# Kernel optimization log

Hardware: AMD Instinct MI355X
Metric: run time of the kernel (lower is better)

The kernel has to match this reference:

```python
import jax, jax.numpy as jnp
import numpy as np

ALPHA = 0.9
EPS = 1e-6


def setup_inputs() -> dict:
    key = jax.random.key(0)
    k1, k2 = jax.random.split(key)
    T, B, D, n = 4096, 16, 1024, 64
    x = jax.random.normal(k1, (T, B, D), dtype=jnp.float32)
    S = jnp.zeros((B, n, n), dtype=jnp.float32)
    # xavier-uniform-ish scale for each [n, D] block of the fused projection
    bound = np.sqrt(6.0 / (n + D))
    W_kvq = jax.random.uniform(k2, (3 * n, D), dtype=jnp.float32, minval=-bound, maxval=bound)
    return {"x": x, "S": S, "W_kvq": W_kvq}


def _e74_forward(x, S0, W_kvq):
    T, B, D = x.shape
    n = W_kvq.shape[0] // 3
    # fused k, v, q projection: [T, B, 3n]
    proj = jnp.einsum('tbd,nd->tbn', x, W_kvq)
    k_all, v_all, q_all = proj[..., :n], proj[..., n:2 * n], proj[..., 2 * n:]

    def step(S, kvq):
        k, v, q = kvq  # each [B, n]
        k_norm = k / (jnp.linalg.norm(k, axis=-1, keepdims=True) + EPS)
        retrieved = jnp.einsum('bij,bj->bi', S, k_norm)
        delta = v - retrieved
        S = ALPHA * S + delta[:, :, None] * k_norm[:, None, :]
        Sq = jnp.einsum('bij,bj->bi', S, q)
        out = Sq * jax.nn.silu(Sq)
        return S, out

    S_final, outputs = jax.lax.scan(step, S0, (k_all, v_all, q_all))
    return outputs, S_final  # [T, B, n], [B, n, n]


def reference(x, S, W_kvq):
    return _e74_forward(x, S, W_kvq)
```

## Files before the change

### kernel.cpp

```cpp
#include <hip/hip_runtime.h>

#define ALPHA 0.9f
#define EPS 1e-6f
#define LOG2A  (-0.15200309344504995f)
#define A64F   (1.1790184577738583e-3f)

constexpr int T_DIM  = 4096;
constexpr int B_DIM  = 16;
constexpr int D_DIM  = 1024;
constexpr int N_DIM  = 64;
constexpr int NPROJ  = 192;
constexpr int NCHUNK = 64;

typedef float  f32x4   __attribute__((ext_vector_type(4)));
typedef _Float16 f16x8 __attribute__((ext_vector_type(8)));

__device__ __forceinline__ float powA(float e) {
  return exp2f(e * LOG2A);
}
__device__ __forceinline__ float rdlane(float v, int src) {
  return __builtin_bit_cast(float,
      __builtin_amdgcn_readlane(__builtin_bit_cast(int, v), src));
}

__device__ __constant__ float APOW[16] = {
  1.f, 0.9f, 0.81f, 0.729f, 0.6561f, 0.59049f, 0.531441f, 0.4782969f,
  0.43046721f, 0.387420489f, 0.3486784401f, 0.31381059609f,
  0.282429536481f, 0.2541865828329f, 0.22876792454961f, 0.205891132094649f};
__device__ __constant__ float AINV[16] = {
  1.f, 1.1111111111f, 1.2345679012f, 1.3717421125f, 1.5241579028f,
  1.6935087809f, 1.8816764232f, 2.0907515814f, 2.3230573126f,
  2.5811747918f, 2.8679719909f, 3.1866355454f, 3.5407061616f,
  3.9341179573f, 4.3712421748f, 4.8569357498f};

__global__ __launch_bounds__(256) void convert_w(
    const float* __restrict__ W, _Float16* __restrict__ w16)
{
  int i = blockIdx.x * 256 + threadIdx.x;
  int c = i >> 10, k = i & 1023;
  w16[(k >> 5) * (NPROJ * 32) + c * 32 + (k & 31)] = (_Float16)W[i];
}

constexpr int BM = 128, BK = 32, NS = D_DIM / BK;

__global__ __launch_bounds__(512, 2) void proj_gemm(
    const float* __restrict__ x, const _Float16* __restrict__ w16,
    _Float16* __restrict__ pf16)
{
  __shared__ _Float16 As[2][BM * BK];
  __shared__ _Float16 Bs[2][NPROJ * BK];
  __shared__ float    nrm[BM][2];

  const int tid  = threadIdx.x;
  const int w    = tid >> 6, lane = tid & 63;
  const int wr   = w >> 2, wc = w & 3;
  const int fr   = lane & 15, fg = lane >> 4;
  const int row0 = blockIdx.x * BM;

  const int arow = tid >> 2, akq = (tid & 3) * 8;
  const float* aSrc = x + (size_t)(row0 + arow) * D_DIM + akq;

  f32x4 acc[4][3];
#pragma unroll
  for (int i = 0; i < 4; ++i)
#pragma unroll
    for (int j = 0; j < 3; ++j) acc[i][j] = (f32x4){0.f, 0.f, 0.f, 0.f};

  float4 a0, a1;

  auto loadA = [&](int s) {
    const float* p = aSrc + s * BK;
    a0 = *(const float4*)p;
    a1 = *(const float4*)(p + 4);
  };
  auto writeA = [&](int buf) {
    f16x8 h;
    h[0] = (_Float16)a0.x; h[1] = (_Float16)a0.y;
    h[2] = (_Float16)a0.z; h[3] = (_Float16)a0.w;
    h[4] = (_Float16)a1.x; h[5] = (_Float16)a1.y;
    h[6] = (_Float16)a1.z; h[7] = (_Float16)a1.w;
    *(f16x8*)&As[buf][arow * BK + akq] = h;
  };
  auto stageB = [&](int buf, int s) {
#pragma unroll
    for (int j = 0; j < 2; ++j) {
      const int sl = j * 8 + w;
      if (sl < 12) {
        const _Float16* src = w16 + (size_t)s * (NPROJ * 32) + sl * 512;
        __builtin_amdgcn_global_load_lds(
            (const __attribute__((address_space(1))) unsigned int*)(src) + lane * 4,
            (__attribute__((address_space(3))) unsigned int*)&Bs[buf][sl * 512],
            16, 0, 0);
      }
    }
  };
  auto compute = [&](int buf) {
    f16x8 af[4];
#pragma unroll
    for (int ar = 0; ar < 4; ++ar)
      af[ar] = *(const f16x8*)&As[buf][(wr * 64 + ar * 16 + fr) * BK + fg * 8];
#pragma unroll
    for (int bc = 0; bc < 3; ++bc) {
      f16x8 bf = *(const f16x8*)&Bs[buf][(wc * 48 + bc * 16 + fr) * BK + fg * 8];
#pragma unroll
      for (int ar = 0; ar < 4; ++ar)
        acc[ar][bc] = __builtin_amdgcn_mfma_f32_16x16x32_f16(af[ar], bf, acc[ar][bc], 0, 0, 0);
    }
  };

  loadA(0);
  stageB(0, 0);
  writeA(0);
  __syncthreads();

  int buf = 0;
  for (int s = 0; s < NS; ++s) {
    if (s + 1 < NS) {
      loadA(s + 1);
      stageB(buf ^ 1, s + 1);
    }
    compute(buf);
    if (s + 1 < NS) writeA(buf ^ 1);
    __syncthreads();
    buf ^= 1;
  }

  if (wc < 2) {
#pragma unroll
    for (int ar = 0; ar < 4; ++ar)
#pragma unroll
      for (int r = 0; r < 4; ++r) {
        float ss;
        if (wc == 0) {
          const float p0 = acc[ar][0][r], p1 = acc[ar][1][r], p2 = acc[ar][2][r];
          ss = p0 * p0 + p1 * p1 + p2 * p2;
        } else {
          const float p0 = acc[ar][0][r];
          ss = p0 * p0;
        }
        ss += __shfl_xor(ss, 1, 64);
        ss += __shfl_xor(ss, 2, 64);
        ss += __shfl_xor(ss, 4, 64);
        ss += __shfl_xor(ss, 8, 64);
        if (fr == 0) nrm[wr * 64 + ar * 16 + fg * 4 + r][wc] = ss;
      }
  }
  __syncthreads();
  if (wc < 2) {
#pragma unroll
    for (int ar = 0; ar < 4; ++ar)
#pragma unroll
      for (int r = 0; r < 4; ++r) {
        const int row = wr * 64 + ar * 16 + fg * 4 + r;
        const float rn = 1.0f / (sqrtf(nrm[row][0] + nrm[row][1]) + EPS);
        if (wc == 0) {
          acc[ar][0][r] *= rn; acc[ar][1][r] *= rn; acc[ar][2][r] *= rn;
        } else {
          acc[ar][0][r] *= rn;
        }
      }
  }

#pragma unroll
  for (int ar = 0; ar < 4; ++ar) {
    const int row = row0 + wr * 64 + ar * 16 + fg * 4;
#pragma unroll
    for (int bc = 0; bc < 3; ++bc) {
      const int col = wc * 48 + bc * 16 + fr;
#pragma unroll
      for (int r = 0; r < 4; ++r)
        pf16[(size_t)(row + r) * NPROJ + col] = (_Float16)acc[ar][bc][r];
    }
  }
}

__global__ __launch_bounds__(64) void scan_sw(
    const _Float16* __restrict__ pf16, const float* __restrict__ S0,
    float* __restrict__ out, float* __restrict__ Sfin)
{
  __shared__ __align__(16) _Float16 sK[64][72];
  __shared__ __align__(16) _Float16 sQ[64][72];
  __shared__ __align__(16) _Float16 sV[64][72];
  __shared__ __align__(16) _Float16 sSW[64][72];
  __shared__ __align__(16) _Float16 sDT[64][80];
  __shared__ __align__(16) _Float16 sBB[16][72];
  __shared__ __align__(16) _Float16 sGt[16][40];

  const int lane = threadIdx.x;
  const int fr = lane & 15, fg = lane >> 4;
  const int b = blockIdx.x & (B_DIM - 1), c = blockIdx.x >> 4;
  const int t0o = c * 64;
  const bool c0 = (c == 0);

#pragma unroll
  for (int j = 0; j < 40; ++j) ((unsigned*)&sDT[0][0])[j * 64 + lane] = 0u;
#pragma unroll
  for (int j = 0; j < 5; ++j) ((unsigned*)&sGt[0][0])[j * 64 + lane] = 0u;

  auto stage64 = [&](_Float16 (*dst)[72], int t0, int sel) {
#pragma unroll
    for (int it = 0; it < 8; ++it) {
      int g = it * 64 + lane, t = g >> 3, c8 = g & 7;
      uint4 v = *(const uint4*)(pf16 + ((size_t)(t0 + t) * B_DIM + b) * NPROJ + sel + c8 * 8);
      *(uint4*)&dst[t][c8 * 8] = v;
    }
  };

  auto dotT = [&](const _Float16* A, int sa, int ra, const _Float16* B, int sb, int rb) {
    f32x4 a = (f32x4){0.f, 0.f, 0.f, 0.f};
    f16x8 af = *(const f16x8*)(A + (ra + fr) * sa + fg * 8);
    f16x8 bf = *(const f16x8*)(B + (rb + fr) * sb + fg * 8);
    a = __builtin_amdgcn_mfma_f32_16x16x32_f16(af, bf, a, 0, 0, 0);
    af = *(const f16x8*)(A + (ra + fr) * sa + 32 + fg * 8);
    bf = *(const f16x8*)(B + (rb + fr) * sb + 32 + fg * 8);
    a = __builtin_amdgcn_mfma_f32_16x16x32_f16(af, bf, a, 0, 0, 0);
    return a;
  };

  auto transposeK = [&]() {
    f16x8 rv[8];
#pragma unroll
    for (int q8 = 0; q8 < 8; ++q8) rv[q8] = *(const f16x8*)&sK[lane][q8 * 8];
#pragma unroll
    for (int q8 = 0; q8 < 8; ++q8)
#pragma unroll
      for (int e = 0; e < 8; ++e) sQ[q8 * 8 + e][lane] = rv[q8][e];
  };

  auto solve = [&](bool isW) {
    for (int k = 0; k < 4; ++k) {
      if (k > 0) {
        f32x4 bacc[4];
#pragma unroll
        for (int ib = 0; ib < 4; ++ib) bacc[ib] = (f32x4){0.f, 0.f, 0.f, 0.f};
        for (int j = 0; j < k; ++j) {
          f32x4 g = dotT(&sK[0][0], 72, k * 16, &sK[0][0], 72, j * 16);
#pragma unroll
          for (int r = 0; r < 4; ++r) {
            const int tl = fg * 4 + r;
            const float e = isW ? (float)(16 * k + tl - 64)
                                : (float)(16 * (k - j) + tl - fr - 1);
            sGt[tl][fr] = (_Float16)(g[r] * powA(e));
          }
#pragma unroll
          for (int ib = 0; ib < 4; ++ib) {
            f16x8 af = *(const f16x8*)&sGt[fr][fg * 8];
            f16x8 bf = *(const f16x8*)&sDT[ib * 16 + fr][j * 16 + fg * 8];
            bacc[ib] = __builtin_amdgcn_mfma_f32_16x16x32_f16(af, bf, bacc[ib], 0, 0, 0);
          }
        }
#pragma unroll
        for (int ib = 0; ib < 4; ++ib)
#pragma unroll
          for (int r = 0; r < 4; ++r)
            sBB[fg * 4 + r][ib * 16 + fr] = (_Float16)bacc[ib][r];
      }

      const f32x4 gd = dotT(&sK[0][0], 72, k * 16, &sK[0][0], 72, k * 16);

      float d[16], dA[16];
#pragma unroll
      for (int t = 0; t < 16; ++t) {
        float base = (float)sV[k * 16 + t][lane];
        if (k > 0) base -= (float)sBB[t][lane];
        float sum = 0.f;
#pragma unroll
        for (int tau = 0; tau < t; ++tau)
          sum = fmaf(rdlane(gd[t & 3], (t >> 2) * 16 + tau), dA[tau], sum);
        d[t] = (t == 0) ? base : fmaf(-APOW[t - 1], sum, base);
        dA[t] = d[t] * AINV[t];
      }
#pragma unroll
      for (int t8 = 0; t8 < 2; ++t8) {
        f16x8 pack;
#pragma unroll
        for (int e = 0; e < 8; ++e) {
          const int tl = t8 * 8 + e;
          const float sc = isW ? powA((float)(63 - (16 * k + tl))) : 1.f;
          pack[e] = (_Float16)(d[tl] * sc);
        }
        *(f16x8*)&sDT[lane][k * 16 + t8 * 8] = pack;
      }
    }
  };

  if (!c0) {
    stage64(sK, t0o - 64, 0);
    stage64(sV, t0o - 64, 64);
    solve(true);
    transposeK();
#pragma unroll
    for (int ti = 0; ti < 4; ++ti)
#pragma unroll
      for (int tj = 0; tj < 4; ++tj) {
        f32x4 a = dotT(&sDT[0][0], 80, ti * 16, &sQ[0][0], 72, tj * 16);
#pragma unroll
        for (int r = 0; r < 4; ++r)
          sSW[ti * 16 + fg * 4 + r][tj * 16 + fr] = (_Float16)a[r];
      }
  } else {
#pragma unroll
    for (int it = 0; it < 8; ++it) {
      const int row = it * 8 + (lane >> 3), col = (lane & 7) * 8;
      const float* src = S0 + (size_t)b * 4096 + row * 64 + col;
      const float4 v1 = *(const float4*)src;
      const float4 v2 = *(const float4*)(src + 4);
      f16x8 pk;
      pk[0] = (_Float16)v1.x; pk[1] = (_Float16)v1.y;
      pk[2] = (_Float16)v1.z; pk[3] = (_Float16)v1.w;
      pk[4] = (_Float16)v2.x; pk[5] = (_Float16)v2.y;
      pk[6] = (_Float16)v2.z; pk[7] = (_Float16)v2.w;
      *(f16x8*)&sSW[row][col] = pk;
    }
  }

  stage64(sK, t0o, 0);
  stage64(sQ, t0o, 128);
  stage64(sV, t0o, 64);

#pragma unroll
  for (int ti = 0; ti < 4; ++ti)
#pragma unroll
    for (int tj = 0; tj < 4; ++tj) {
      f32x4 a = dotT(&sK[0][0], 72, ti * 16, &sSW[0][0], 72, tj * 16);
#pragma unroll
      for (int r = 0; r < 4; ++r) {
        const int t = ti * 16 + fg * 4 + r, i = tj * 16 + fr;
        const float vo = (float)sV[t][i];
        sV[t][i] = (_Float16)(vo - powA((float)t) * a[r]);
      }
    }

  f32x4 sq[16];
#pragma unroll
  for (int ti = 0; ti < 4; ++ti)
#pragma unroll
    for (int tj = 0; tj < 4; ++tj) {
      f32x4 a = dotT(&sQ[0][0], 72, ti * 16, &sSW[0][0], 72, tj * 16);
#pragma unroll
      for (int r = 0; r < 4; ++r)
        a[r] *= powA((float)(ti * 16 + fg * 4 + r + 1));
      sq[ti * 4 + tj] = a;
    }

  solve(false);

#pragma unroll
  for (int tb = 0; tb < 4; ++tb)
#pragma unroll
    for (int qb = 0; qb < 4; ++qb) {
      if (qb <= tb) {
        f32x4 h = dotT(&sQ[0][0], 72, tb * 16, &sK[0][0], 72, qb * 16);
#pragma unroll
        for (int r = 0; r < 4; ++r) {
          const int tl = fg * 4 + r;
          const int t = tb * 16 + tl, tau = qb * 16 + fr;
          const float val = (tau <= t) ? h[r] * powA((float)(t - tau)) : 0.f;
          sGt[tl][fr] = (_Float16)val;
        }
#pragma unroll
        for (int ib = 0; ib < 4; ++ib) {
          f16x8 af = *(const f16x8*)&sGt[fr][fg * 8];
          f16x8 bf = *(const f16x8*)&sDT[ib * 16 + fr][qb * 16 + fg * 8];
          sq[tb * 4 + ib] = __builtin_amdgcn_mfma_f32_16x16x32_f16(af, bf, sq[tb * 4 + ib], 0, 0, 0);
        }
      }
    }

#pragma unroll
  for (int ti = 0; ti < 4; ++ti)
#pragma unroll
    for (int tj = 0; tj < 4; ++tj)
#pragma unroll
      for (int r = 0; r < 4; ++r) {
        const int t = ti * 16 + fg * 4 + r, i = tj * 16 + fr;
        const float Sq = sq[ti * 4 + tj][r];
        const float sig = 1.0f / (1.0f + __expf(-Sq));
        out[(size_t)(t0o + t) * 1024 + b * 64 + i] = Sq * Sq * sig;
      }

  if (c == NCHUNK - 1) {
#pragma unroll
    for (int t8 = 0; t8 < 8; ++t8) {
      f16x8 v = *(const f16x8*)&sDT[lane][t8 * 8];
#pragma unroll
      for (int e = 0; e < 8; ++e)
        v[e] = (_Float16)((float)v[e] * powA((float)(63 - (t8 * 8 + e))));
      *(f16x8*)&sDT[lane][t8 * 8] = v;
    }
    transposeK();
#pragma unroll
    for (int ti = 0; ti < 4; ++ti)
#pragma unroll
      for (int tj = 0; tj < 4; ++tj) {
        f32x4 so = dotT(&sDT[0][0], 80, ti * 16, &sQ[0][0], 72, tj * 16);
#pragma unroll
        for (int r = 0; r < 4; ++r) {
          const int i = ti * 16 + fg * 4 + r, j = tj * 16 + fr;
          Sfin[((size_t)b * 64 + i) * 64 + j] = A64F * (float)sSW[i][j] + so[r];
        }
      }
  }
}

extern "C" void kernel_launch(void* const* d_in, const int* in_sizes, int n_in,
                              void* d_out, int out_size, void* d_ws, size_t ws_size,
                              hipStream_t stream)
{
  const float* x  = (const float*)d_in[0];
  const float* S0 = (const float*)d_in[1];
  const float* Wk = (const float*)d_in[2];
  float* out  = (float*)d_out;
  float* Sfin = out + (size_t)T_DIM * B_DIM * N_DIM;

  char* wsb = (char*)d_ws;
  _Float16* pf16 = (_Float16*)(wsb);
  _Float16* w16  = (_Float16*)(wsb + 25165824);

  convert_w<<<(NPROJ * D_DIM) / 256, 256, 0, stream>>>(Wk, w16);
  proj_gemm<<<(T_DIM * B_DIM) / BM, 512, 0, stream>>>(x, w16, pf16);
  scan_sw<<<B_DIM * NCHUNK, 64, 0, stream>>>(pf16, S0, out, Sfin);
}
```

Before: 120.3 us.

## Stage GEMM epilogue through LDS and shrink scan kernel LDS and registers

The projection GEMM now stages its fp16 output tile through shared memory, reusing the operand buffers, so each thread writes 16-byte vectors instead of scattered 2-byte stores. In the scan kernel, V is read straight from global memory into registers inside the solve, and the K·S correction is folded into each solve block. Q is staged in two 32-row halves, the K transpose is done in place, and the output accumulators are kept per 16-row block instead of all 16 tiles. The forward-substitution dot product is split across four partial sums to shorten the dependency chain. Together these cut LDS footprint and register pressure to raise occupancy, at the cost of extra barriers and global loads inside the serial solve.

```diff
diff --git a/kernel.cpp b/kernel.cpp
--- a/kernel.cpp
+++ b/kernel.cpp
@@ -47,9 +47,12 @@
     const float* __restrict__ x, const _Float16* __restrict__ w16,
     _Float16* __restrict__ pf16)
 {
-  __shared__ _Float16 As[2][BM * BK];
-  __shared__ _Float16 Bs[2][NPROJ * BK];
-  __shared__ float    nrm[BM][2];
+  __shared__ __align__(16) _Float16 smem[2 * BM * BK + 2 * NPROJ * BK];
+  __shared__ float nrm[BM][2];
+
+  _Float16 (*As)[BM * BK]    = (_Float16(*)[BM * BK])smem;
+  _Float16 (*Bs)[NPROJ * BK] = (_Float16(*)[NPROJ * BK])(smem + 2 * BM * BK);
+  _Float16 (*ep)[200]        = (_Float16(*)[200])smem;
 
   const int tid  = threadIdx.x;
   const int w    = tid >> 6, lane = tid & 63;
@@ -162,14 +165,24 @@
   }
 
 #pragma unroll
-  for (int ar = 0; ar < 4; ++ar) {
-    const int row = row0 + wr * 64 + ar * 16 + fg * 4;
-#pragma unroll
-    for (int bc = 0; bc < 3; ++bc) {
-      const int col = wc * 48 + bc * 16 + fr;
-#pragma unroll
-      for (int r = 0; r < 4; ++r)
-        pf16[(size_t)(row + r) * NPROJ + col] = (_Float16)acc[ar][bc][r];
+  for (int p = 0; p < 2; ++p) {
+    __syncthreads();
+    if (wr == p) {
+#pragma unroll
+      for (int ar = 0; ar < 4; ++ar)
+#pragma unroll
+        for (int bc = 0; bc < 3; ++bc)
+#pragma unroll
+          for (int r = 0; r < 4; ++r)
+            ep[ar * 16 + fg * 4 + r][wc * 48 + bc * 16 + fr] = (_Float16)acc[ar][bc][r];
+    }
+    __syncthreads();
+#pragma unroll
+    for (int u = 0; u < 3; ++u) {
+      const int g = u * 512 + tid;
+      const int rr = g / 24, cc = g - rr * 24;
+      *(f16x8*)(pf16 + (size_t)(row0 + p * 64 + rr) * NPROJ + cc * 8) =
+          *(const f16x8*)&ep[rr][cc * 8];
     }
   }
 }
@@ -179,12 +192,11 @@
     float* __restrict__ out, float* __restrict__ Sfin)
 {
   __shared__ __align__(16) _Float16 sK[64][72];
-  __shared__ __align__(16) _Float16 sQ[64][72];
-  __shared__ __align__(16) _Float16 sV[64][72];
+  __shared__ __align__(16) _Float16 sQ[32][72];
   __shared__ __align__(16) _Float16 sSW[64][72];
-  __shared__ __align__(16) _Float16 sDT[64][80];
+  __shared__ __align__(16) _Float16 sDT[64][72];
   __shared__ __align__(16) _Float16 sBB[16][72];
-  __shared__ __align__(16) _Float16 sGt[16][40];
+  __shared__ __align__(16) _Float16 uGt[16][72];
 
   const int lane = threadIdx.x;
   const int fr = lane & 15, fg = lane >> 4;
@@ -193,9 +205,9 @@
   const bool c0 = (c == 0);
 
 #pragma unroll
-  for (int j = 0; j < 40; ++j) ((unsigned*)&sDT[0][0])[j * 64 + lane] = 0u;
-#pragma unroll
-  for (int j = 0; j < 5; ++j) ((unsigned*)&sGt[0][0])[j * 64 + lane] = 0u;
+  for (int u = 0; u < 36; ++u) ((unsigned*)&sDT[0][0])[u * 64 + lane] = 0u;
+#pragma unroll
+  for (int u = 0; u < 9; ++u) ((unsigned*)&uGt[0][0])[u * 64 + lane] = 0u;
 
   auto stage64 = [&](_Float16 (*dst)[72], int t0, int sel) {
 #pragma unroll
@@ -203,6 +215,15 @@
       int g = it * 64 + lane, t = g >> 3, c8 = g & 7;
       uint4 v = *(const uint4*)(pf16 + ((size_t)(t0 + t) * B_DIM + b) * NPROJ + sel + c8 * 8);
       *(uint4*)&dst[t][c8 * 8] = v;
+    }
+  };
+  auto stageQ = [&](int half) {
+#pragma unroll
+    for (int it = 0; it < 4; ++it) {
+      int g = it * 64 + lane, t = g >> 3, c8 = g & 7;
+      uint4 v = *(const uint4*)(pf16 +
+          ((size_t)(t0o + half * 32 + t) * B_DIM + b) * NPROJ + 128 + c8 * 8);
+      *(uint4*)&sQ[t][c8 * 8] = v;
     }
   };
 
@@ -221,14 +242,21 @@
     f16x8 rv[8];
 #pragma unroll
     for (int q8 = 0; q8 < 8; ++q8) rv[q8] = *(const f16x8*)&sK[lane][q8 * 8];
+    asm volatile("" ::: "memory");
 #pragma unroll
     for (int q8 = 0; q8 < 8; ++q8)
 #pragma unroll
-      for (int e = 0; e < 8; ++e) sQ[q8 * 8 + e][lane] = rv[q8][e];
-  };
-
-  auto solve = [&](bool isW) {
+      for (int e = 0; e < 8; ++e) sK[q8 * 8 + e][lane] = rv[q8][e];
+  };
+
+  auto solve = [&](bool isW, int t0v) {
+#pragma unroll
     for (int k = 0; k < 4; ++k) {
+      _Float16 vr[16];
+#pragma unroll
+      for (int t = 0; t < 16; ++t)
+        vr[t] = pf16[((size_t)(t0v + k * 16 + t) * B_DIM + b) * NPROJ + 64 + lane];
+
       if (k > 0) {
         f32x4 bacc[4];
 #pragma unroll
@@ -240,11 +268,11 @@
             const int tl = fg * 4 + r;
             const float e = isW ? (float)(16 * k + tl - 64)
                                 : (float)(16 * (k - j) + tl - fr - 1);
-            sGt[tl][fr] = (_Float16)(g[r] * powA(e));
+            uGt[tl][fr] = (_Float16)(g[r] * powA(e));
           }
 #pragma unroll
           for (int ib = 0; ib < 4; ++ib) {
-            f16x8 af = *(const f16x8*)&sGt[fr][fg * 8];
+            f16x8 af = *(const f16x8*)&uGt[fr][fg * 8];
             f16x8 bf = *(const f16x8*)&sDT[ib * 16 + fr][j * 16 + fg * 8];
             bacc[ib] = __builtin_amdgcn_mfma_f32_16x16x32_f16(af, bf, bacc[ib], 0, 0, 0);
           }
@@ -258,15 +286,33 @@
 
       const f32x4 gd = dotT(&sK[0][0], 72, k * 16, &sK[0][0], 72, k * 16);
 
+      if (!isW) {
+#pragma unroll
+        for (int tj = 0; tj < 4; ++tj) {
+          f32x4 a = dotT(&sK[0][0], 72, k * 16, &sSW[0][0], 72, tj * 16);
+#pragma unroll
+          for (int r = 0; r < 4; ++r)
+            uGt[fg * 4 + r][tj * 16 + fr] =
+                (_Float16)(a[r] * powA((float)(16 * k + fg * 4 + r)));
+        }
+      }
+
       float d[16], dA[16];
 #pragma unroll
       for (int t = 0; t < 16; ++t) {
-        float base = (float)sV[k * 16 + t][lane];
+        float base = (float)vr[t];
+        if (!isW) base -= (float)uGt[t][lane];
         if (k > 0) base -= (float)sBB[t][lane];
-        float sum = 0.f;
-#pragma unroll
-        for (int tau = 0; tau < t; ++tau)
-          sum = fmaf(rdlane(gd[t & 3], (t >> 2) * 16 + tau), dA[tau], sum);
+        float p0 = 0.f, p1 = 0.f, p2 = 0.f, p3 = 0.f;
+#pragma unroll
+        for (int tau = 0; tau < t; ++tau) {
+          const float gv = rdlane(gd[t & 3], (t >> 2) * 16 + tau);
+          if ((tau & 3) == 0)      p0 = fmaf(gv, dA[tau], p0);
+          else if ((tau & 3) == 1) p1 = fmaf(gv, dA[tau], p1);
+          else if ((tau & 3) == 2) p2 = fmaf(gv, dA[tau], p2);
+          else                     p3 = fmaf(gv, dA[tau], p3);
+        }
+        const float sum = (p0 + p1) + (p2 + p3);
         d[t] = (t == 0) ? base : fmaf(-APOW[t - 1], sum, base);
         dA[t] = d[t] * AINV[t];
       }
@@ -281,19 +327,26 @@
         }
         *(f16x8*)&sDT[lane][k * 16 + t8 * 8] = pack;
       }
+
+      if (!isW) {
+#pragma unroll
+        for (int u = 0; u < 2; ++u) {
+          const int idx = lane * 2 + u;
+          *((unsigned*)&uGt[idx >> 3][16] + (idx & 7)) = 0u;
+        }
+      }
     }
   };
 
   if (!c0) {
     stage64(sK, t0o - 64, 0);
-    stage64(sV, t0o - 64, 64);
-    solve(true);
+    solve(true, t0o - 64);
     transposeK();
 #pragma unroll
     for (int ti = 0; ti < 4; ++ti)
 #pragma unroll
       for (int tj = 0; tj < 4; ++tj) {
-        f32x4 a = dotT(&sDT[0][0], 80, ti * 16, &sQ[0][0], 72, tj * 16);
+        f32x4 a = dotT(&sDT[0][0], 72, ti * 16, &sK[0][0], 72, tj * 16);
 #pragma unroll
         for (int r = 0; r < 4; ++r)
           sSW[ti * 16 + fg * 4 + r][tj * 16 + fr] = (_Float16)a[r];
@@ -315,69 +368,51 @@
   }
 
   stage64(sK, t0o, 0);
-  stage64(sQ, t0o, 128);
-  stage64(sV, t0o, 64);
-
-#pragma unroll
-  for (int ti = 0; ti < 4; ++ti)
-#pragma unroll
-    for (int tj = 0; tj < 4; ++tj) {
-      f32x4 a = dotT(&sK[0][0], 72, ti * 16, &sSW[0][0], 72, tj * 16);
-#pragma unroll
-      for (int r = 0; r < 4; ++r) {
-        const int t = ti * 16 + fg * 4 + r, i = tj * 16 + fr;
-        const float vo = (float)sV[t][i];
-        sV[t][i] = (_Float16)(vo - powA((float)t) * a[r]);
-      }
-    }
-
-  f32x4 sq[16];
-#pragma unroll
-  for (int ti = 0; ti < 4; ++ti)
-#pragma unroll
-    for (int tj = 0; tj < 4; ++tj) {
-      f32x4 a = dotT(&sQ[0][0], 72, ti * 16, &sSW[0][0], 72, tj * 16);
-#pragma unroll
-      for (int r = 0; r < 4; ++r)
-        a[r] *= powA((float)(ti * 16 + fg * 4 + r + 1));
-      sq[ti * 4 + tj] = a;
-    }
-
-  solve(false);
-
-#pragma unroll
-  for (int tb = 0; tb < 4; ++tb)
-#pragma unroll
-    for (int qb = 0; qb < 4; ++qb) {
-      if (qb <= tb) {
-        f32x4 h = dotT(&sQ[0][0], 72, tb * 16, &sK[0][0], 72, qb * 16);
+  stageQ(0);
+  solve(false, t0o);
+
+#pragma unroll
+  for (int h2 = 0; h2 < 2; ++h2) {
+    if (h2) stageQ(1);
+#pragma unroll
+    for (int tb2 = 0; tb2 < 2; ++tb2) {
+      const int tb = h2 * 2 + tb2;
+      f32x4 sq[4];
+#pragma unroll
+      for (int tj = 0; tj < 4; ++tj) {
+        f32x4 a = dotT(&sQ[0][0], 72, tb2 * 16, &sSW[0][0], 72, tj * 16);
+#pragma unroll
+        for (int r = 0; r < 4; ++r)
+          a[r] *= powA((float)(tb * 16 + fg * 4 + r + 1));
+        sq[tj] = a;
+      }
+      for (int qb = 0; qb <= tb; ++qb) {
+        f32x4 h = dotT(&sQ[0][0], 72, tb2 * 16, &sK[0][0], 72, qb * 16);
 #pragma unroll
         for (int r = 0; r < 4; ++r) {
           const int tl = fg * 4 + r;
           const int t = tb * 16 + tl, tau = qb * 16 + fr;
           const float val = (tau <= t) ? h[r] * powA((float)(t - tau)) : 0.f;
-          sGt[tl][fr] = (_Float16)val;
+          uGt[tl][fr] = (_Float16)val;
         }
 #pragma unroll
         for (int ib = 0; ib < 4; ++ib) {
-          f16x8 af = *(const f16x8*)&sGt[fr][fg * 8];
+          f16x8 af = *(const f16x8*)&uGt[fr][fg * 8];
           f16x8 bf = *(const f16x8*)&sDT[ib * 16 + fr][qb * 16 + fg * 8];
-          sq[tb * 4 + ib] = __builtin_amdgcn_mfma_f32_16x16x32_f16(af, bf, sq[tb * 4 + ib], 0, 0, 0);
-        }
-      }
-    }
-
-#pragma unroll
-  for (int ti = 0; ti < 4; ++ti)
-#pragma unroll
-    for (int tj = 0; tj < 4; ++tj)
-#pragma unroll
-      for (int r = 0; r < 4; ++r) {
-        const int t = ti * 16 + fg * 4 + r, i = tj * 16 + fr;
-        const float Sq = sq[ti * 4 + tj][r];
-        const float sig = 1.0f / (1.0f + __expf(-Sq));
-        out[(size_t)(t0o + t) * 1024 + b * 64 + i] = Sq * Sq * sig;
-      }
+          sq[ib] = __builtin_amdgcn_mfma_f32_16x16x32_f16(af, bf, sq[ib], 0, 0, 0);
+        }
+      }
+#pragma unroll
+      for (int tj = 0; tj < 4; ++tj)
+#pragma unroll
+        for (int r = 0; r < 4; ++r) {
+          const int t = tb * 16 + fg * 4 + r, i = tj * 16 + fr;
+          const float Sq = sq[tj][r];
+          const float sig = 1.0f / (1.0f + __expf(-Sq));
+          out[(size_t)(t0o + t) * 1024 + b * 64 + i] = Sq * Sq * sig;
+        }
+    }
+  }
 
   if (c == NCHUNK - 1) {
 #pragma unroll
@@ -393,7 +428,7 @@
     for (int ti = 0; ti < 4; ++ti)
 #pragma unroll
       for (int tj = 0; tj < 4; ++tj) {
-        f32x4 so = dotT(&sDT[0][0], 80, ti * 16, &sQ[0][0], 72, tj * 16);
+        f32x4 so = dotT(&sDT[0][0], 72, ti * 16, &sK[0][0], 72, tj * 16);
 #pragma unroll
         for (int r = 0; r < 4; ++r) {
           const int i = ti * 16 + fg * 4 + r, j = tj * 16 + fr;
```

Result: faster. 106.0 us (-11.9%).
